# Kernel optimization log

Measured on AMD Instinct MI355X. Metric: run time of the kernel, lower is better.

The kernel has to match this reference:

```python
import jax, jax.numpy as jnp
import numpy as np

# ---- static config (eval-mode RPN, torchvision-style FPN) ----
LEVEL_HW = [(200, 200), (100, 100), (50, 50), (25, 25), (13, 13)]
STRIDES = [4, 8, 16, 32, 64]
SIZES = [32, 64, 128, 256, 512]
A = 3                      # anchors per location (3 aspect ratios)
IMG_H, IMG_W = 800, 800
PRE_N, POST_N = 1000, 1000 # pre/post NMS top-n (testing)
NMS_TH, SCORE_TH, MIN_SIZE = 0.7, 0.0, 1e-3
BBOX_CLIP = 4.135166556742356  # log(1000/16), BoxCoder clamp
NUM_PER_LEVEL = [A * h * w for h, w in LEVEL_HW]


def _make_anchors():
    ratios = np.array([0.5, 1.0, 2.0])
    hr = np.sqrt(ratios)
    wr = 1.0 / hr
    out = []
    for (H, W), size, stride in zip(LEVEL_HW, SIZES, STRIDES):
        ws, hs = wr * size, hr * size
        base = np.stack([-ws / 2, -hs / 2, ws / 2, hs / 2], axis=1)  # [A,4]
        sx = np.arange(W) * stride
        sy = np.arange(H) * stride
        yy, xx = np.meshgrid(sy, sx, indexing='ij')
        shifts = np.stack([xx.ravel(), yy.ravel(), xx.ravel(), yy.ravel()], axis=1)
        out.append((shifts[:, None, :] + base[None, :, :]).reshape(-1, 4))
    return np.concatenate(out, 0).astype(np.float32)


def setup_inputs() -> dict:
    key = jax.random.key(0)
    ks = jax.random.split(key, 10)
    N = 4
    inp = {}
    for i, (h, w) in enumerate(LEVEL_HW):
        inp[f'obj{i}'] = jax.random.normal(ks[i], (N, A, h, w), jnp.float32)
        inp[f'delta{i}'] = 0.5 * jax.random.normal(ks[5 + i], (N, 4 * A, h, w), jnp.float32)
    inp['anchors'] = jnp.asarray(_make_anchors())
    return inp


def _decode(deltas, anchors):
    # BoxCoder.decode with weights (1,1,1,1)
    wa = anchors[:, 2] - anchors[:, 0]
    ha = anchors[:, 3] - anchors[:, 1]
    cxa = anchors[:, 0] + 0.5 * wa
    cya = anchors[:, 1] + 0.5 * ha
    dx, dy = deltas[..., 0], deltas[..., 1]
    dw = jnp.minimum(deltas[..., 2], BBOX_CLIP)
    dh = jnp.minimum(deltas[..., 3], BBOX_CLIP)
    cx = dx * wa + cxa
    cy = dy * ha + cya
    w = jnp.exp(dw) * wa
    h = jnp.exp(dh) * ha
    return jnp.stack([cx - 0.5 * w, cy - 0.5 * h, cx + 0.5 * w, cy + 0.5 * h], -1)


def _box_iou(b1, b2):
    a1 = (b1[:, 2] - b1[:, 0]) * (b1[:, 3] - b1[:, 1])
    a2 = (b2[:, 2] - b2[:, 0]) * (b2[:, 3] - b2[:, 1])
    lt = jnp.maximum(b1[:, None, :2], b2[None, :, :2])
    rb = jnp.minimum(b1[:, None, 2:], b2[None, :, 2:])
    wh = jnp.clip(rb - lt, 0.0)
    inter = wh[..., 0] * wh[..., 1]
    return inter / (a1[:, None] + a2[None, :] - inter)


def _nms_keep(iou, valid):
    # greedy NMS over score-sorted boxes; valid marks surviving pre-filters
    K = iou.shape[0]
    def body(sup, i):
        k = valid[i] & jnp.logical_not(sup[i])
        sup = sup | (k & (iou[i] > NMS_TH))
        return sup, k
    _, keeps = jax.lax.scan(body, jnp.zeros(K, bool), jnp.arange(K))
    return keeps


def _per_image(boxes, scores, lvl):
    # clip_boxes_to_image
    x1 = jnp.clip(boxes[:, 0], 0.0, IMG_W)
    y1 = jnp.clip(boxes[:, 1], 0.0, IMG_H)
    x2 = jnp.clip(boxes[:, 2], 0.0, IMG_W)
    y2 = jnp.clip(boxes[:, 3], 0.0, IMG_H)
    boxes = jnp.stack([x1, y1, x2, y2], -1)
    # remove_small_boxes + score_thresh as validity mask
    valid = (x2 - x1 >= MIN_SIZE) & (y2 - y1 >= MIN_SIZE) & (scores >= SCORE_TH)
    ms = jnp.where(valid, scores, -1.0)
    order = jnp.argsort(-ms)
    b_s, v_s, s_s, l_s = boxes[order], valid[order], scores[order], lvl[order]
    # batched_nms trick: offset boxes by level so levels never overlap
    bn = jax.lax.stop_gradient(b_s) + (l_s.astype(boxes.dtype) * (IMG_W + 1.0))[:, None]
    keep = _nms_keep(_box_iou(bn, bn), v_s)
    sel_key = jnp.where(keep, jax.lax.stop_gradient(s_s), -1.0)
    topv, topi = jax.lax.top_k(sel_key, POST_N)
    m = topv > -0.5
    fb = jnp.where(m[:, None], b_s[topi], 0.0)
    fs = jnp.where(m, s_s[topi], 0.0)
    return fb, fs


def reference(obj0, obj1, obj2, obj3, obj4, delta0, delta1, delta2, delta3, delta4, anchors):
    objs = [obj0, obj1, obj2, obj3, obj4]
    dels = [delta0, delta1, delta2, delta3, delta4]
    N = obj0.shape[0]
    # permute_and_flatten + concat (objectness C=1)
    obj = jnp.concatenate([o.transpose(0, 2, 3, 1).reshape(N, -1) for o in objs], 1)
    dl = jnp.concatenate([
        d.reshape(N, A, 4, d.shape[2], d.shape[3]).transpose(0, 3, 4, 1, 2).reshape(N, -1, 4)
        for d in dels], 1)
    proposals = _decode(dl, anchors)  # [N, total, 4]
    levels = jnp.concatenate([jnp.full((n,), i, jnp.int32) for i, n in enumerate(NUM_PER_LEVEL)])
    # per-level top-k (static split)
    idxs, off = [], 0
    for n in NUM_PER_LEVEL:
        k = min(PRE_N, n)
        _, ti = jax.lax.top_k(obj[:, off:off + n], k)
        idxs.append(ti + off)
        off += n
    top_idx = jnp.concatenate(idxs, 1)  # [N, K]
    sel_obj = jnp.take_along_axis(obj, top_idx, 1)
    sel_lvl = levels[top_idx]
    sel_box = jnp.take_along_axis(proposals, top_idx[..., None], 1)
    scores = jax.nn.sigmoid(sel_obj)
    fb, fs = jax.vmap(_per_image)(sel_box, scores, sel_lvl)
    return fb, fs
```

## Files before the change

kernel.cpp:

```cpp
#include <hip/hip_runtime.h>
#include <cstdint>
#include <cstddef>

#define NLV 5
#define NIMG 4
#define NSEL 4507
#define TSEL (NIMG * NSEL)
#define POSTN 1000
#define TCAP 8192
#define TTCAP 2048
#define NHB 16
#define PBLK 64
#define PCH 1875

__device__ const int d_W[NLV]    = {200, 100, 50, 25, 13};
__device__ const int d_NL[NLV]   = {120000, 30000, 7500, 1875, 507};
__device__ const int d_KOFF[6]   = {0, 120000, 150000, 157500, 159375, 159882};
__device__ const int d_LOFF[6]   = {0, 1000, 2000, 3000, 4000, 4507};
__device__ const int d_KL[NLV]   = {1000, 1000, 1000, 1000, 507};

struct Ptrs {
    const float* obj[NLV];
    const float* del[NLV];
    const float* anch;
};

__device__ inline unsigned int dkey_of(float f) {
    unsigned int u = __float_as_uint(f);
    unsigned int mk = (u & 0x80000000u) ? ~u : (u | 0x80000000u);
    return ~mk;
}
__device__ inline float logit_from_dkey(unsigned int dk) {
    unsigned int mk = ~dk;
    unsigned int u = (mk & 0x80000000u) ? (mk & 0x7fffffffu) : ~mk;
    return __uint_as_float(u);
}

__global__ __launch_bounds__(256) void k_hist(Ptrs P, unsigned int* hist) {
    int l = blockIdx.y, n = blockIdx.z;
    int nl_sz = d_NL[l];
    if (d_KL[l] >= nl_sz) return;
    int nlid = n * NLV + l;
    __shared__ unsigned int h[2048];
    for (int i = threadIdx.x; i < 2048; i += 256) h[i] = 0;
    __syncthreads();
    const float* ob = P.obj[l] + (size_t)n * nl_sz;
    int chunk = (nl_sz + NHB - 1) / NHB;
    int beg = blockIdx.x * chunk;
    int end = min(beg + chunk, nl_sz);
    for (int t = beg + (int)threadIdx.x; t < end; t += 256)
        atomicAdd(&h[dkey_of(ob[t]) >> 21], 1u);
    __syncthreads();
    unsigned int* out = hist + ((size_t)nlid * NHB + blockIdx.x) * 2048;
    for (int i = threadIdx.x; i < 2048; i += 256) out[i] = h[i];
}

__global__ __launch_bounds__(1024) void k_thresh(const unsigned int* hist,
                                                 unsigned int* thr,
                                                 int* scnt, int* tcnt) {
    int nlid = blockIdx.x;
    int l = nlid % NLV;
    if (threadIdx.x == 0) { scnt[nlid] = 0; tcnt[nlid] = 0; }
    if (d_KL[l] >= d_NL[l]) return;
    int tid = threadIdx.x, w = tid >> 6, lane = tid & 63;
    __shared__ unsigned int wpre[16];
    const unsigned int* hb = hist + (size_t)nlid * NHB * 2048;
    unsigned int v0 = 0, v1 = 0;
    #pragma unroll
    for (int sh = 0; sh < NHB; ++sh) {
        v0 += hb[sh * 2048 + 2 * tid];
        v1 += hb[sh * 2048 + 2 * tid + 1];
    }
    unsigned int s = v0 + v1;
    unsigned int ps = s;
    #pragma unroll
    for (int d = 1; d < 64; d <<= 1) {
        unsigned int t2 = (unsigned int)__shfl_up((int)ps, d, 64);
        if (lane >= d) ps += t2;
    }
    if (lane == 63) wpre[w] = ps;
    __syncthreads();
    unsigned int base = 0;
    #pragma unroll
    for (int ww = 0; ww < 16; ++ww) if (ww < w) base += wpre[ww];
    unsigned int incl = base + ps;
    unsigned int target = (unsigned int)d_KL[l];
    unsigned int exc0 = incl - s, inc0 = incl - v1;
    unsigned int exc1 = inc0,    inc1 = incl;
    if (exc0 < target && target <= inc0) { thr[nlid * 2] = 2 * tid;     thr[nlid * 2 + 1] = exc0; }
    if (exc1 < target && target <= inc1) { thr[nlid * 2] = 2 * tid + 1; thr[nlid * 2 + 1] = exc1; }
}

__global__ __launch_bounds__(256) void k_pick(Ptrs P, const unsigned int* thr,
                                              int* scnt, int* tcnt,
                                              int* cg, float* cl,
                                              unsigned long long* tiebuf) {
    int l = blockIdx.y, n = blockIdx.z;
    int nl_sz = d_NL[l], kl = d_KL[l];
    int nlid = n * NLV + l;
    const float* ob = P.obj[l] + (size_t)n * nl_sz;
    int cbase = n * NSEL + d_LOFF[l];
    int koff = d_KOFF[l];
    int Wl = d_W[l], HW = Wl * Wl;
    int chunk = (nl_sz + PBLK - 1) / PBLK;
    int beg = blockIdx.x * chunk;
    int end = min(beg + chunk, nl_sz);
    int tid = threadIdx.x;

    if (kl >= nl_sz) {
        for (int t = beg + tid; t < end; t += 256) {
            int a = t / HW, rem = t - a * HW;
            int p = rem * 3 + a;
            cg[cbase + p] = koff + p;
            cl[cbase + p] = ob[t];
        }
        return;
    }
    __shared__ int sp[PCH];
    __shared__ float sl[PCH];
    __shared__ unsigned long long tb[PCH];
    __shared__ int nsel, ntie, sbase, tbase;
    if (tid == 0) { nsel = 0; ntie = 0; }
    __syncthreads();

    unsigned int b0 = thr[nlid * 2];
    for (int t = beg + tid; t < end; t += 256) {
        float lg = ob[t];
        unsigned int dk = dkey_of(lg);
        unsigned int bin = dk >> 21;
        if (bin < b0) {
            int pos = atomicAdd(&nsel, 1);
            int a = t / HW, rem = t - a * HW;
            sp[pos] = rem * 3 + a;
            sl[pos] = lg;
        } else if (bin == b0) {
            int pos = atomicAdd(&ntie, 1);
            int a = t / HW, rem = t - a * HW;
            tb[pos] = ((unsigned long long)dk << 17) |
                      (unsigned long long)(unsigned int)(rem * 3 + a);
        }
    }
    __syncthreads();
    if (tid == 0) {
        sbase = atomicAdd(&scnt[nlid], nsel);
        tbase = atomicAdd(&tcnt[nlid], ntie);
    }
    __syncthreads();
    int ns = nsel, nt = ntie, sb = sbase, tbs = tbase;
    for (int i = tid; i < ns; i += 256) {
        cg[cbase + sb + i] = koff + sp[i];
        cl[cbase + sb + i] = sl[i];
    }
    for (int i = tid; i < nt; i += 256) {
        int slot = tbs + i;
        if (slot < TCAP) tiebuf[(size_t)nlid * TCAP + slot] = tb[i];
    }
}

__global__ __launch_bounds__(1024) void k_tbs(Ptrs P, const unsigned int* thr,
                                              const int* tcnt,
                                              const unsigned long long* tiebuf,
                                              int* cg, float* cl,
                                              unsigned long long* skey,
                                              float4* sboxL, float* slogL,
                                              int* ccnt) {
#pragma clang fp contract(off)
    __shared__ union {
        struct { unsigned long long kk[TCAP];
                 unsigned long long tt[TTCAP];
                 unsigned int h2[2048]; } tie;
        struct { unsigned long long s[1024];
                 float4 bx[1024];
                 float lg[1024]; } srt;
    } U;
    __shared__ unsigned int wpre[16];
    __shared__ unsigned int s_b1, s_before;
    __shared__ int ctr, ttc;

    int l = blockIdx.x, n = blockIdx.y;
    int nl = n * NLV + l;
    int tid = threadIdx.x, w = tid >> 6, lane = tid & 63;
    int kl = d_KL[l], nl_sz = d_NL[l];
    int cbase = n * NSEL + d_LOFF[l];
    int koff = d_KOFF[l];

    if (kl < nl_sz) {
        int c = min(tcnt[nl], TCAP);
        unsigned int cnt_lt = thr[nl * 2 + 1];
        int need = kl - (int)cnt_lt;
        if (tid == 0) { ctr = 0; ttc = 0; }
        U.tie.h2[tid] = 0; U.tie.h2[tid + 1024] = 0;
        for (int i = tid; i < c; i += 1024) U.tie.kk[i] = tiebuf[(size_t)nl * TCAP + i];
        __syncthreads();
        for (int i = tid; i < c; i += 1024)
            atomicAdd(&U.tie.h2[(unsigned int)((U.tie.kk[i] >> 27) & 0x7ffull)], 1u);
        __syncthreads();
        unsigned int v0 = U.tie.h2[2 * tid], v1 = U.tie.h2[2 * tid + 1];
        unsigned int s = v0 + v1, ps = s;
        #pragma unroll
        for (int d = 1; d < 64; d <<= 1) {
            unsigned int t2 = (unsigned int)__shfl_up((int)ps, d, 64);
            if (lane >= d) ps += t2;
        }
        if (lane == 63) wpre[w] = ps;
        __syncthreads();
        unsigned int base = 0;
        #pragma unroll
        for (int ww = 0; ww < 16; ++ww) if (ww < w) base += wpre[ww];
        unsigned int incl = base + ps;
        unsigned int target = (unsigned int)need;
        unsigned int exc0 = incl - s, inc0 = incl - v1;
        unsigned int exc1 = inc0,    inc1 = incl;
        if (exc0 < target && target <= inc0) { s_b1 = 2 * tid;     s_before = exc0; }
        if (exc1 < target && target <= inc1) { s_b1 = 2 * tid + 1; s_before = exc1; }
        __syncthreads();
        unsigned int b1 = s_b1;
        int before = (int)s_before;
        for (int i = tid; i < c; i += 1024) {
            unsigned long long ki = U.tie.kk[i];
            unsigned int sb = (unsigned int)((ki >> 27) & 0x7ffull);
            if (sb < b1) {
                int slot = atomicAdd(&ctr, 1);
                int p = (int)(ki & 0x1ffffull);
                cg[cbase + (int)cnt_lt + slot] = koff + p;
                cl[cbase + (int)cnt_lt + slot] = logit_from_dkey((unsigned int)(ki >> 17));
            } else if (sb == b1) {
                int j = atomicAdd(&ttc, 1);
                if (j < TTCAP) U.tie.tt[j] = ki;
            }
        }
        __syncthreads();
        int c2 = min(ttc, TTCAP);
        int need2 = need - before;
        for (int i = tid; i < c2; i += 1024) {
            unsigned long long ki = U.tie.tt[i];
            int rank = 0;
            for (int j = 0; j < c2; ++j) rank += (U.tie.tt[j] < ki) ? 1 : 0;
            if (rank < need2) {
                int p = (int)(ki & 0x1ffffull);
                cg[cbase + (int)cnt_lt + before + rank] = koff + p;
                cl[cbase + (int)cnt_lt + before + rank] = logit_from_dkey((unsigned int)(ki >> 17));
            }
        }
    }
    __syncthreads();

    {
        int j = tid;
        unsigned long long key;
        float4 box;
        float lgv;
        if (j >= kl) {
            key = ((unsigned long long)0xFFFFFFFFu << 27) | (unsigned long long)j;
            box = make_float4(0.f, 0.f, 0.f, 0.f);
            lgv = 0.f;
        } else {
            int sidx = cbase + j;
            int gidx = cg[sidx];
            float lg = cl[sidx];
            int p = gidx - koff;
            int Wl = d_W[l];
            int HW = Wl * Wl;
            int a = p % 3, hw = p / 3;
            int hq = hw / Wl, wq = hw - hq * Wl;
            const float* dl = P.del[l];
            size_t dbase = (size_t)(n * 12 + a * 4) * HW + (size_t)hq * Wl + wq;
            float dx = dl[dbase], dy = dl[dbase + HW];
            float dw = dl[dbase + 2 * (size_t)HW], dh = dl[dbase + 3 * (size_t)HW];
            const float* an = P.anch + 4 * (size_t)gidx;
            float ax1 = an[0], ay1 = an[1], ax2 = an[2], ay2 = an[3];
            float wa = ax2 - ax1, ha = ay2 - ay1;
            float cxa = ax1 + 0.5f * wa, cya = ay1 + 0.5f * ha;
            const float CLIPC = (float)4.135166556742356;
            dw = fminf(dw, CLIPC); dh = fminf(dh, CLIPC);
            float cx = dx * wa + cxa;
            float cy = dy * ha + cya;
            float ww2 = expf(dw) * wa;
            float hh2 = expf(dh) * ha;
            float x1 = cx - 0.5f * ww2, y1 = cy - 0.5f * hh2;
            float x2 = cx + 0.5f * ww2, y2 = cy + 0.5f * hh2;
            x1 = fminf(fmaxf(x1, 0.0f), 800.0f);
            y1 = fminf(fmaxf(y1, 0.0f), 800.0f);
            x2 = fminf(fmaxf(x2, 0.0f), 800.0f);
            y2 = fminf(fmaxf(y2, 0.0f), 800.0f);
            bool valid = (x2 - x1 >= 1e-3f) && (y2 - y1 >= 1e-3f);
            box = make_float4(x1, y1, x2, y2);
            lgv = lg;
            unsigned int sk = valid ? dkey_of(lg) : 0xffffffffu;
            key = ((unsigned long long)sk << 27) |
                  ((unsigned long long)(unsigned int)p << 10) | (unsigned long long)j;
        }
        U.srt.s[j] = key;
        U.srt.bx[j] = box;
        U.srt.lg[j] = lgv;
    }
    __syncthreads();

    for (int k = 2; k <= 1024; k <<= 1) {
        for (int j2 = k >> 1; j2 > 0; j2 >>= 1) {
            if (tid < 512) {
                int i = ((tid & ~(j2 - 1)) << 1) | (tid & (j2 - 1));
                int ix = i | j2;
                bool up = ((i & k) == 0);
                unsigned long long A = U.srt.s[i], B = U.srt.s[ix];
                if ((A > B) == up) { U.srt.s[i] = B; U.srt.s[ix] = A; }
            }
            __syncthreads();
        }
    }
    {
        int e = tid;
        unsigned long long key = U.srt.s[e];
        int j = (int)(key & 0x3ffull);
        skey[(size_t)nl * 1024 + e] = key;
        sboxL[(size_t)nl * 1024 + e] = U.srt.bx[j];
        slogL[(size_t)nl * 1024 + e] = U.srt.lg[j];
        bool v = (key >> 27) != 0xFFFFFFFFull;
        bool vn = (e < 1023) ? ((U.srt.s[e + 1] >> 27) != 0xFFFFFFFFull) : false;
        if (e == 0 && !v) ccnt[nl] = 0;
        if (v && (e == 1023 || !vn)) ccnt[nl] = e + 1;
    }
}

__global__ __launch_bounds__(256) void k_mask(const float4* sboxL, const int* ccnt,
                                              unsigned long long* MT) {
#pragma clang fp contract(off)
    int n = blockIdx.z, l = blockIdx.y;
    int ci = blockIdx.x >> 4, cj = blockIdx.x & 15;
    int nl = n * NLV + l;
    int cnt = ccnt[nl];
    int nw = (cnt + 63) / 64;
    if (cj < ci || cj >= nw) return;
    __shared__ float4 bi[64], bj[64];
    int tid = threadIdx.x;
    float off = (float)l * 801.0f;
    if (tid < 64) {
        float4 b = sboxL[nl * 1024 + cj * 64 + tid];
        bj[tid] = make_float4(b.x + off, b.y + off, b.z + off, b.w + off);
    } else if (tid < 128) {
        float4 b = sboxL[nl * 1024 + ci * 64 + (tid - 64)];
        bi[tid - 64] = make_float4(b.x + off, b.y + off, b.z + off, b.w + off);
    }
    __syncthreads();
    int w = tid >> 6, lane = tid & 63;
    float4 B = bj[lane];
    float a2 = (B.z - B.x) * (B.w - B.y);
    unsigned long long* outp = MT + ((size_t)nl * 16 + cj) * 1024 + ci * 64;
    #pragma unroll
    for (int t = 0; t < 16; ++t) {
        int i = w * 16 + t;
        float4 A = bi[i];
        float a1 = (A.z - A.x) * (A.w - A.y);
        float ltx = fmaxf(A.x, B.x), lty = fmaxf(A.y, B.y);
        float rbx = fminf(A.z, B.z), rby = fminf(A.w, B.w);
        float wx = fmaxf(rbx - ltx, 0.f), wy = fmaxf(rby - lty, 0.f);
        float inter = wx * wy;
        float iou = inter / ((a1 + a2) - inter);
        unsigned long long word = __ballot(iou > 0.7f);
        if (lane == 0) outp[i] = word;
    }
}

__global__ __launch_bounds__(1024) void k_scan(const unsigned long long* MT,
                                               const int* ccnt,
                                               unsigned long long* keepL,
                                               float* out) {
    int l = blockIdx.x, n = blockIdx.y;
    int nl = n * NLV + l;
    int tid = threadIdx.x, w = tid >> 6, lane = tid & 63;
    __shared__ unsigned long long pendS[16];
    __shared__ unsigned long long defS[16];
    {
        int seg = POSTN / NLV;
        for (int i = tid; i < seg; i += 1024) {
            int idx = n * POSTN + l * seg + i;
            ((float4*)out)[idx] = make_float4(0.f, 0.f, 0.f, 0.f);
            out[NIMG * POSTN * 4 + idx] = 0.f;
        }
    }
    int cnt = ccnt[nl];
    int nw = (cnt + 63) / 64;

    const unsigned long long* base = MT + ((size_t)nl * 16 + w) * 1024;
    unsigned long long Dmask = 0;
    if (w < nw)
        Dmask = base[(size_t)w * 64 + lane] & ~((2ull << lane) - 1ull);
    unsigned long long rows[15];
    #pragma unroll
    for (int cc = 0; cc < 15; ++cc)
        rows[cc] = (cc < w && w < nw) ? base[(size_t)cc * 64 + lane] : 0ull;

    int nb = max(0, min(64, cnt - w * 64));
    unsigned long long pend_w = (nb == 64) ? ~0ull : ((nb > 0) ? ((1ull << nb) - 1ull) : 0ull);
    unsigned long long K_w = 0;
    if (lane == 0) pendS[w] = pend_w;
    __syncthreads();

    for (int round = 0; round < 1024; ++round) {
        unsigned long long any = 0;
        #pragma unroll
        for (int cc = 0; cc < 16; ++cc) any |= pendS[cc];
        if (!any) break;
        unsigned long long acc = ((pendS[w] >> lane) & 1ull) ? Dmask : 0ull;
        #pragma unroll
        for (int cc = 0; cc < 15; ++cc)
            if (cc < w) acc |= ((pendS[cc] >> lane) & 1ull) ? rows[cc] : 0ull;
        unsigned int vlo = (unsigned int)acc, vhi = (unsigned int)(acc >> 32);
        #pragma unroll
        for (int m = 1; m < 64; m <<= 1) {
            vlo |= (unsigned int)__shfl_xor((int)vlo, m, 64);
            vhi |= (unsigned int)__shfl_xor((int)vhi, m, 64);
        }
        unsigned long long sup = ((unsigned long long)vhi << 32) | (unsigned long long)vlo;
        unsigned long long def_w = pend_w & ~sup;
        K_w |= def_w;
        if (lane == 0) defS[w] = def_w;
        __syncthreads();
        unsigned long long acc2 = ((defS[w] >> lane) & 1ull) ? Dmask : 0ull;
        #pragma unroll
        for (int cc = 0; cc < 15; ++cc)
            if (cc < w) acc2 |= ((defS[cc] >> lane) & 1ull) ? rows[cc] : 0ull;
        unsigned int rlo = (unsigned int)acc2, rhi = (unsigned int)(acc2 >> 32);
        #pragma unroll
        for (int m = 1; m < 64; m <<= 1) {
            rlo |= (unsigned int)__shfl_xor((int)rlo, m, 64);
            rhi |= (unsigned int)__shfl_xor((int)rhi, m, 64);
        }
        unsigned long long rem = ((unsigned long long)rhi << 32) | (unsigned long long)rlo;
        pend_w &= ~def_w & ~rem;
        if (lane == 0) pendS[w] = pend_w;
        __syncthreads();
    }
    if (lane == 0) keepL[nl * 16 + w] = K_w;
}

__global__ __launch_bounds__(1024) void k_rank(const unsigned long long* skey,
                                               const unsigned long long* keepL,
                                               const int* ccnt,
                                               const float4* sboxL, const float* slogL,
                                               float* out) {
    int l = blockIdx.x, n = blockIdx.y;
    int tid = threadIdx.x;
    __shared__ unsigned long long KS[NLV][1024];
    __shared__ unsigned long long kd[NLV][16];
    __shared__ int kpre[NLV][17];
    __shared__ int lcnt[NLV];
    for (int e = tid; e < NLV * 1024; e += 1024)
        ((unsigned long long*)KS)[e] = skey[(size_t)n * NLV * 1024 + e];
    if (tid < NLV * 16) ((unsigned long long*)kd)[tid] = keepL[n * NLV * 16 + tid];
    if (tid < NLV) lcnt[tid] = ccnt[n * NLV + tid];
    __syncthreads();
    if (tid < NLV) {
        int run = 0;
        for (int q = 0; q < 16; ++q) { kpre[tid][q] = run; run += (int)__popcll(kd[tid][q]); }
        kpre[tid][16] = run;
    }
    __syncthreads();
    int i = tid;
    if (i >= lcnt[l]) return;
    int q = i >> 6, b = i & 63;
    if (!((kd[l][q] >> b) & 1ull)) return;
    int rank = kpre[l][q] + (int)__popcll(kd[l][q] & ((1ull << b) - 1ull));
    unsigned int sk = (unsigned int)(KS[l][i] >> 27);
    for (int l2 = 0; l2 < NLV; ++l2) {
        if (l2 == l) continue;
        int c2 = lcnt[l2];
        unsigned long long bound = (l2 < l)
            ? (((unsigned long long)sk + 1ull) << 27)
            : ((unsigned long long)sk << 27);
        int lo = 0, hi = c2;
        while (lo < hi) {
            int mid = (lo + hi) >> 1;
            if (KS[l2][mid] < bound) lo = mid + 1; else hi = mid;
        }
        int mq = lo >> 6, mb = lo & 63;
        rank += kpre[l2][mq] + (mb ? (int)__popcll(kd[l2][mq] & ((1ull << mb) - 1ull)) : 0);
    }
    if (rank < POSTN) {
        ((float4*)out)[n * POSTN + rank] = sboxL[(size_t)(n * NLV + l) * 1024 + i];
        float lg = slogL[(size_t)(n * NLV + l) * 1024 + i];
        out[NIMG * POSTN * 4 + n * POSTN + rank] = 1.0f / (1.0f + expf(-lg));
    }
}

extern "C" void kernel_launch(void* const* d_in, const int* in_sizes, int n_in,
                              void* d_out, int out_size, void* d_ws, size_t ws_size,
                              hipStream_t stream) {
    Ptrs P;
    bool interleaved = (in_sizes[1] == 4 * in_sizes[0]);
    for (int i = 0; i < NLV; ++i) {
        if (interleaved) {
            P.obj[i] = (const float*)d_in[2 * i];
            P.del[i] = (const float*)d_in[2 * i + 1];
        } else {
            P.obj[i] = (const float*)d_in[i];
            P.del[i] = (const float*)d_in[NLV + i];
        }
    }
    P.anch = (const float*)d_in[10];

    char* w = (char*)d_ws;
    size_t off = 0;
    auto alloc = [&](size_t bytes) {
        void* p = w + off;
        off = (off + bytes + 255) & ~(size_t)255;
        return p;
    };
    const size_t NLT = (size_t)NIMG * NLV * 1024;
    unsigned int* hist = (unsigned int*)alloc((size_t)NIMG * NLV * NHB * 2048 * 4);
    int* scnt = (int*)alloc(256);
    int* tcnt = (int*)alloc(256);
    unsigned int* thr = (unsigned int*)alloc((size_t)NIMG * NLV * 2 * 4);
    unsigned long long* tiebuf = (unsigned long long*)alloc((size_t)NIMG * NLV * TCAP * 8);
    int* cg      = (int*)alloc((size_t)TSEL * 4);
    float* cl    = (float*)alloc((size_t)TSEL * 4);
    unsigned long long* skey = (unsigned long long*)alloc(NLT * 8);
    float4* sboxL = (float4*)alloc(NLT * 16);
    float* slogL  = (float*)alloc(NLT * 4);
    int* ccnt    = (int*)alloc((size_t)NIMG * NLV * 4);
    unsigned long long* keepL = (unsigned long long*)alloc((size_t)NIMG * NLV * 16 * 8);
    unsigned long long* MT = (unsigned long long*)alloc((size_t)NIMG * NLV * 16 * 1024 * 8);
    (void)ws_size; (void)n_in;

    k_hist<<<dim3(NHB, NLV, NIMG), 256, 0, stream>>>(P, hist);
    k_thresh<<<NIMG * NLV, 1024, 0, stream>>>(hist, thr, scnt, tcnt);
    k_pick<<<dim3(PBLK, NLV, NIMG), 256, 0, stream>>>(P, thr, scnt, tcnt, cg, cl, tiebuf);
    k_tbs<<<dim3(NLV, NIMG), 1024, 0, stream>>>(P, thr, tcnt, tiebuf, cg, cl,
                                                skey, sboxL, slogL, ccnt);
    k_mask<<<dim3(256, NLV, NIMG), 256, 0, stream>>>(sboxL, ccnt, MT);
    k_scan<<<dim3(NLV, NIMG), 1024, 0, stream>>>(MT, ccnt, keepL, (float*)d_out);
    k_rank<<<dim3(NLV, NIMG), 1024, 0, stream>>>(skey, keepL, ccnt, sboxL, slogL, (float*)d_out);
}
```

Measured before the change: 159.7 us.

## Fuse seven RPN kernels into one cooperative persistent kernel with grid syncs

Replaces the chain of seven kernel launches (histogram, threshold, pick, tie-break sort, IoU mask, NMS scan, rank) with a single cooperative kernel of 256 blocks x 1024 threads that separates the phases with grid-wide syncs. The goal is to remove per-launch overhead and the gaps between small dependent kernels. Work is remapped onto fixed block counts: the histogram packs four sub-blocks per block, pick runs in five passes, and the IoU mask uses a loop over triangle tiles. The old multi-launch path is kept as a fallback if the cooperative launch fails. The cost is that grid syncs add their own latency, and the 1024-thread blocks with a large shared-memory union may limit occupancy in the phases that do most of the work.

```diff
diff --git a/kernel.cpp b/kernel.cpp
--- a/kernel.cpp
+++ b/kernel.cpp
@@ -1,6 +1,9 @@
 #include <hip/hip_runtime.h>
+#include <hip/hip_cooperative_groups.h>
 #include <cstdint>
 #include <cstddef>
+
+namespace cgrp = cooperative_groups;
 
 #define NLV 5
 #define NIMG 4
@@ -12,6 +15,8 @@
 #define NHB 16
 #define PBLK 64
 #define PCH 1875
+#define NTRI 136
+#define GRID 256
 
 __device__ const int d_W[NLV]    = {200, 100, 50, 25, 13};
 __device__ const int d_NL[NLV]   = {120000, 30000, 7500, 1875, 507};
@@ -34,6 +39,450 @@
     unsigned int mk = ~dk;
     unsigned int u = (mk & 0x80000000u) ? (mk & 0x7fffffffu) : ~mk;
     return __uint_as_float(u);
+}
+
+__global__ __launch_bounds__(1024) void k_all(Ptrs P,
+        unsigned int* hist, int* scnt, int* tcnt, unsigned int* thr,
+        unsigned long long* tiebuf, int* cgv, float* clv,
+        unsigned long long* skey, float4* sboxL, float* slogL,
+        int* ccnt, unsigned long long* keepL, unsigned long long* MT,
+        float* out) {
+#pragma clang fp contract(off)
+    cgrp::grid_group gg = cgrp::this_grid();
+    int bid = blockIdx.x, tid = threadIdx.x;
+    int w = tid >> 6, lane = tid & 63;
+
+    __shared__ union {
+        unsigned int h4[4][2048];
+        struct { int sp[PCH]; float sl[PCH];
+                 unsigned long long tb[PCH]; } pk;
+        struct { unsigned long long kk[TCAP];
+                 unsigned long long tt[TTCAP];
+                 unsigned int h2[2048]; } tie;
+        struct { unsigned long long s[1024]; float4 bx[1024];
+                 float lg[1024]; } srt;
+        struct { float4 bi[64]; float4 bj[64]; } mk;
+        unsigned long long KS[NLV][1024];
+    } U;
+    __shared__ unsigned int wpre[16];
+    __shared__ unsigned int s_b1, s_before;
+    __shared__ int ctr, ttc;
+    __shared__ int nselS, ntieS, sbaseS, tbaseS;
+    __shared__ unsigned long long pendS[16], defS[16];
+    __shared__ unsigned long long kd[NLV][16];
+    __shared__ int kpre[NLV][17];
+    __shared__ int lcnt[NLV];
+
+    {
+        for (int i = tid; i < 4 * 2048; i += 1024) ((unsigned int*)U.h4)[i] = 0;
+        __syncthreads();
+        int g = bid * 4 + (tid >> 8);
+        int tsub = tid & 255;
+        int u = ((g % 3) == 0 && (g / 3) < 320) ? (g / 3) : -1;
+        int nlid = -1, l = 0, n = 0, sub = 0;
+        if (u >= 0) {
+            nlid = u >> 4; sub = u & 15;
+            n = nlid / NLV; l = nlid % NLV;
+            if (d_KL[l] >= d_NL[l]) nlid = -1;
+        }
+        if (nlid >= 0) {
+            int nl_sz = d_NL[l];
+            const float* ob = P.obj[l] + (size_t)n * nl_sz;
+            int chunk = (nl_sz + NHB - 1) / NHB;
+            int beg = sub * chunk, end = min(beg + chunk, nl_sz);
+            unsigned int* hh = U.h4[tid >> 8];
+            for (int t = beg + tsub; t < end; t += 256)
+                atomicAdd(&hh[dkey_of(ob[t]) >> 21], 1u);
+        }
+        __syncthreads();
+        if (nlid >= 0) {
+            unsigned int* hh = U.h4[tid >> 8];
+            unsigned int* op = hist + ((size_t)nlid * NHB + sub) * 2048;
+            for (int i = tsub; i < 2048; i += 256) op[i] = hh[i];
+        }
+        if (bid >= GRID - 16) {
+            int z = (bid - (GRID - 16)) * 1024 + tid;
+            if (z < NIMG * POSTN) {
+                ((float4*)out)[z] = make_float4(0.f, 0.f, 0.f, 0.f);
+                out[NIMG * POSTN * 4 + z] = 0.f;
+            }
+        }
+    }
+    gg.sync();
+
+    if (bid < NIMG * NLV) {
+        int nlid = bid, l = nlid % NLV;
+        if (tid == 0) { scnt[nlid] = 0; tcnt[nlid] = 0; }
+        if (d_KL[l] < d_NL[l]) {
+            const unsigned int* hb = hist + (size_t)nlid * NHB * 2048;
+            unsigned int v0 = 0, v1 = 0;
+            #pragma unroll
+            for (int sh = 0; sh < NHB; ++sh) {
+                v0 += hb[sh * 2048 + 2 * tid];
+                v1 += hb[sh * 2048 + 2 * tid + 1];
+            }
+            unsigned int s = v0 + v1, ps = s;
+            #pragma unroll
+            for (int d = 1; d < 64; d <<= 1) {
+                unsigned int t2 = (unsigned int)__shfl_up((int)ps, d, 64);
+                if (lane >= d) ps += t2;
+            }
+            if (lane == 63) wpre[w] = ps;
+            __syncthreads();
+            unsigned int base = 0;
+            #pragma unroll
+            for (int ww = 0; ww < 16; ++ww) if (ww < w) base += wpre[ww];
+            unsigned int incl = base + ps;
+            unsigned int target = (unsigned int)d_KL[l];
+            unsigned int exc0 = incl - s, inc0 = incl - v1;
+            unsigned int exc1 = inc0,    inc1 = incl;
+            if (exc0 < target && target <= inc0) { thr[nlid * 2] = 2 * tid;     thr[nlid * 2 + 1] = exc0; }
+            if (exc1 < target && target <= inc1) { thr[nlid * 2] = 2 * tid + 1; thr[nlid * 2 + 1] = exc1; }
+        }
+    }
+    gg.sync();
+
+    for (int pass = 0; pass < 5; ++pass) {
+        int unit = pass * GRID + bid;
+        int nlid = unit >> 6, pb = unit & 63;
+        int n = nlid / NLV, l = nlid % NLV;
+        int nl_sz = d_NL[l], kl = d_KL[l];
+        const float* ob = P.obj[l] + (size_t)n * nl_sz;
+        int cbase = n * NSEL + d_LOFF[l];
+        int koff = d_KOFF[l];
+        int Wl = d_W[l], HW = Wl * Wl;
+        int chunk = (nl_sz + PBLK - 1) / PBLK;
+        int beg = pb * chunk, end = min(beg + chunk, nl_sz);
+
+        if (kl >= nl_sz) {
+            for (int t = beg + tid; t < end; t += 1024) {
+                int a = t / HW, rem = t - a * HW;
+                int p = rem * 3 + a;
+                cgv[cbase + p] = koff + p;
+                clv[cbase + p] = ob[t];
+            }
+            continue;
+        }
+        if (tid == 0) { nselS = 0; ntieS = 0; }
+        __syncthreads();
+        unsigned int b0 = thr[nlid * 2];
+        for (int t = beg + tid; t < end; t += 1024) {
+            float lg = ob[t];
+            unsigned int dk = dkey_of(lg);
+            unsigned int bin = dk >> 21;
+            if (bin < b0) {
+                int pos = atomicAdd(&nselS, 1);
+                int a = t / HW, rem = t - a * HW;
+                U.pk.sp[pos] = rem * 3 + a;
+                U.pk.sl[pos] = lg;
+            } else if (bin == b0) {
+                int pos = atomicAdd(&ntieS, 1);
+                int a = t / HW, rem = t - a * HW;
+                U.pk.tb[pos] = ((unsigned long long)dk << 17) |
+                               (unsigned long long)(unsigned int)(rem * 3 + a);
+            }
+        }
+        __syncthreads();
+        if (tid == 0) {
+            sbaseS = atomicAdd(&scnt[nlid], nselS);
+            tbaseS = atomicAdd(&tcnt[nlid], ntieS);
+        }
+        __syncthreads();
+        int ns = nselS, nt2 = ntieS, sb = sbaseS, tb2 = tbaseS;
+        for (int i = tid; i < ns; i += 1024) {
+            cgv[cbase + sb + i] = koff + U.pk.sp[i];
+            clv[cbase + sb + i] = U.pk.sl[i];
+        }
+        for (int i = tid; i < nt2; i += 1024) {
+            int slot = tb2 + i;
+            if (slot < TCAP) tiebuf[(size_t)nlid * TCAP + slot] = U.pk.tb[i];
+        }
+    }
+    gg.sync();
+
+    if (bid < NIMG * NLV) {
+        int nlid = bid;
+        int n = nlid / NLV, l = nlid % NLV;
+        int kl = d_KL[l], nl_sz = d_NL[l];
+        int cbase = n * NSEL + d_LOFF[l];
+        int koff = d_KOFF[l];
+
+        if (kl < nl_sz) {
+            int c = min(tcnt[nlid], TCAP);
+            unsigned int cnt_lt = thr[nlid * 2 + 1];
+            int need = kl - (int)cnt_lt;
+            if (tid == 0) { ctr = 0; ttc = 0; }
+            U.tie.h2[tid] = 0; U.tie.h2[tid + 1024] = 0;
+            for (int i = tid; i < c; i += 1024) U.tie.kk[i] = tiebuf[(size_t)nlid * TCAP + i];
+            __syncthreads();
+            for (int i = tid; i < c; i += 1024)
+                atomicAdd(&U.tie.h2[(unsigned int)((U.tie.kk[i] >> 27) & 0x7ffull)], 1u);
+            __syncthreads();
+            unsigned int v0 = U.tie.h2[2 * tid], v1 = U.tie.h2[2 * tid + 1];
+            unsigned int s = v0 + v1, ps = s;
+            #pragma unroll
+            for (int d = 1; d < 64; d <<= 1) {
+                unsigned int t2 = (unsigned int)__shfl_up((int)ps, d, 64);
+                if (lane >= d) ps += t2;
+            }
+            if (lane == 63) wpre[w] = ps;
+            __syncthreads();
+            unsigned int base = 0;
+            #pragma unroll
+            for (int ww = 0; ww < 16; ++ww) if (ww < w) base += wpre[ww];
+            unsigned int incl = base + ps;
+            unsigned int target = (unsigned int)need;
+            unsigned int exc0 = incl - s, inc0 = incl - v1;
+            unsigned int exc1 = inc0,    inc1 = incl;
+            if (exc0 < target && target <= inc0) { s_b1 = 2 * tid;     s_before = exc0; }
+            if (exc1 < target && target <= inc1) { s_b1 = 2 * tid + 1; s_before = exc1; }
+            __syncthreads();
+            unsigned int b1 = s_b1;
+            int before = (int)s_before;
+            for (int i = tid; i < c; i += 1024) {
+                unsigned long long ki = U.tie.kk[i];
+                unsigned int sb = (unsigned int)((ki >> 27) & 0x7ffull);
+                if (sb < b1) {
+                    int slot = atomicAdd(&ctr, 1);
+                    int p = (int)(ki & 0x1ffffull);
+                    cgv[cbase + (int)cnt_lt + slot] = koff + p;
+                    clv[cbase + (int)cnt_lt + slot] = logit_from_dkey((unsigned int)(ki >> 17));
+                } else if (sb == b1) {
+                    int j = atomicAdd(&ttc, 1);
+                    if (j < TTCAP) U.tie.tt[j] = ki;
+                }
+            }
+            __syncthreads();
+            int c2 = min(ttc, TTCAP);
+            int need2 = need - before;
+            for (int i = tid; i < c2; i += 1024) {
+                unsigned long long ki = U.tie.tt[i];
+                int rank = 0;
+                for (int j = 0; j < c2; ++j) rank += (U.tie.tt[j] < ki) ? 1 : 0;
+                if (rank < need2) {
+                    int p = (int)(ki & 0x1ffffull);
+                    cgv[cbase + (int)cnt_lt + before + rank] = koff + p;
+                    clv[cbase + (int)cnt_lt + before + rank] = logit_from_dkey((unsigned int)(ki >> 17));
+                }
+            }
+        }
+        __syncthreads();
+
+        {
+            int j = tid;
+            unsigned long long key;
+            float4 box;
+            float lgv;
+            if (j >= kl) {
+                key = ((unsigned long long)0xFFFFFFFFu << 27) | (unsigned long long)j;
+                box = make_float4(0.f, 0.f, 0.f, 0.f);
+                lgv = 0.f;
+            } else {
+                int sidx = cbase + j;
+                int gidx = cgv[sidx];
+                float lg = clv[sidx];
+                int p = gidx - koff;
+                int Wl = d_W[l];
+                int HW = Wl * Wl;
+                int a = p % 3, hw = p / 3;
+                int hq = hw / Wl, wq = hw - hq * Wl;
+                const float* dl = P.del[l];
+                size_t dbase = (size_t)(n * 12 + a * 4) * HW + (size_t)hq * Wl + wq;
+                float dx = dl[dbase], dy = dl[dbase + HW];
+                float dw = dl[dbase + 2 * (size_t)HW], dh = dl[dbase + 3 * (size_t)HW];
+                const float* an = P.anch + 4 * (size_t)gidx;
+                float ax1 = an[0], ay1 = an[1], ax2 = an[2], ay2 = an[3];
+                float wa = ax2 - ax1, ha = ay2 - ay1;
+                float cxa = ax1 + 0.5f * wa, cya = ay1 + 0.5f * ha;
+                const float CLIPC = (float)4.135166556742356;
+                dw = fminf(dw, CLIPC); dh = fminf(dh, CLIPC);
+                float cx = dx * wa + cxa;
+                float cy = dy * ha + cya;
+                float ww2 = expf(dw) * wa;
+                float hh2 = expf(dh) * ha;
+                float x1 = cx - 0.5f * ww2, y1 = cy - 0.5f * hh2;
+                float x2 = cx + 0.5f * ww2, y2 = cy + 0.5f * hh2;
+                x1 = fminf(fmaxf(x1, 0.0f), 800.0f);
+                y1 = fminf(fmaxf(y1, 0.0f), 800.0f);
+                x2 = fminf(fmaxf(x2, 0.0f), 800.0f);
+                y2 = fminf(fmaxf(y2, 0.0f), 800.0f);
+                bool valid = (x2 - x1 >= 1e-3f) && (y2 - y1 >= 1e-3f);
+                box = make_float4(x1, y1, x2, y2);
+                lgv = lg;
+                unsigned int sk = valid ? dkey_of(lg) : 0xffffffffu;
+                key = ((unsigned long long)sk << 27) |
+                      ((unsigned long long)(unsigned int)p << 10) | (unsigned long long)j;
+            }
+            U.srt.s[j] = key;
+            U.srt.bx[j] = box;
+            U.srt.lg[j] = lgv;
+        }
+        __syncthreads();
+
+        for (int k = 2; k <= 1024; k <<= 1) {
+            for (int j2 = k >> 1; j2 > 0; j2 >>= 1) {
+                if (tid < 512) {
+                    int i = ((tid & ~(j2 - 1)) << 1) | (tid & (j2 - 1));
+                    int ix = i | j2;
+                    bool up = ((i & k) == 0);
+                    unsigned long long A = U.srt.s[i], B = U.srt.s[ix];
+                    if ((A > B) == up) { U.srt.s[i] = B; U.srt.s[ix] = A; }
+                }
+                __syncthreads();
+            }
+        }
+        {
+            int e = tid;
+            unsigned long long key = U.srt.s[e];
+            int j = (int)(key & 0x3ffull);
+            skey[(size_t)nlid * 1024 + e] = key;
+            sboxL[(size_t)nlid * 1024 + e] = U.srt.bx[j];
+            slogL[(size_t)nlid * 1024 + e] = U.srt.lg[j];
+            bool v = (key >> 27) != 0xFFFFFFFFull;
+            bool vn = (e < 1023) ? ((U.srt.s[e + 1] >> 27) != 0xFFFFFFFFull) : false;
+            if (e == 0 && !v) ccnt[nlid] = 0;
+            if (v && (e == 1023 || !vn)) ccnt[nlid] = e + 1;
+        }
+    }
+    gg.sync();
+
+    for (int T = bid; T < NIMG * NLV * NTRI; T += GRID) {
+        int nl = T / NTRI, t136 = T - nl * NTRI;
+        int cnt = ccnt[nl];
+        int nw = (cnt + 63) / 64;
+        int cj = 0;
+        while (((cj + 1) * (cj + 2)) >> 1 <= t136) ++cj;
+        int ci = t136 - ((cj * (cj + 1)) >> 1);
+        if (cj >= nw) continue;
+        int l = nl % NLV;
+        float off = (float)l * 801.0f;
+        __syncthreads();
+        if (tid < 64) {
+            float4 b = sboxL[(size_t)nl * 1024 + cj * 64 + tid];
+            U.mk.bj[tid] = make_float4(b.x + off, b.y + off, b.z + off, b.w + off);
+        } else if (tid < 128) {
+            float4 b = sboxL[(size_t)nl * 1024 + ci * 64 + (tid - 64)];
+            U.mk.bi[tid - 64] = make_float4(b.x + off, b.y + off, b.z + off, b.w + off);
+        }
+        __syncthreads();
+        float4 B = U.mk.bj[lane];
+        float a2 = (B.z - B.x) * (B.w - B.y);
+        unsigned long long* outp = MT + ((size_t)nl * 16 + cj) * 1024 + ci * 64;
+        #pragma unroll
+        for (int t = 0; t < 4; ++t) {
+            int i = w * 4 + t;
+            float4 A = U.mk.bi[i];
+            float a1 = (A.z - A.x) * (A.w - A.y);
+            float ltx = fmaxf(A.x, B.x), lty = fmaxf(A.y, B.y);
+            float rbx = fminf(A.z, B.z), rby = fminf(A.w, B.w);
+            float wx = fmaxf(rbx - ltx, 0.f), wy = fmaxf(rby - lty, 0.f);
+            float inter = wx * wy;
+            float iou = inter / ((a1 + a2) - inter);
+            unsigned long long word = __ballot(iou > 0.7f);
+            if (lane == 0) outp[i] = word;
+        }
+    }
+    gg.sync();
+
+    if (bid < NIMG * NLV) {
+        int nl = bid;
+        int cnt = ccnt[nl];
+        int nw = (cnt + 63) / 64;
+        const unsigned long long* base = MT + ((size_t)nl * 16 + w) * 1024;
+        unsigned long long Dmask = 0;
+        if (w < nw)
+            Dmask = base[(size_t)w * 64 + lane] & ~((2ull << lane) - 1ull);
+        unsigned long long rows[15];
+        #pragma unroll
+        for (int cc = 0; cc < 15; ++cc)
+            rows[cc] = (cc < w && w < nw) ? base[(size_t)cc * 64 + lane] : 0ull;
+
+        int nb = max(0, min(64, cnt - w * 64));
+        unsigned long long pend_w = (nb == 64) ? ~0ull : ((nb > 0) ? ((1ull << nb) - 1ull) : 0ull);
+        unsigned long long K_w = 0;
+        if (lane == 0) pendS[w] = pend_w;
+        __syncthreads();
+
+        for (int round = 0; round < 1024; ++round) {
+            unsigned long long any = 0;
+            #pragma unroll
+            for (int cc = 0; cc < 16; ++cc) any |= pendS[cc];
+            if (!any) break;
+            unsigned long long acc = ((pendS[w] >> lane) & 1ull) ? Dmask : 0ull;
+            #pragma unroll
+            for (int cc = 0; cc < 15; ++cc)
+                if (cc < w) acc |= ((pendS[cc] >> lane) & 1ull) ? rows[cc] : 0ull;
+            unsigned int vlo = (unsigned int)acc, vhi = (unsigned int)(acc >> 32);
+            #pragma unroll
+            for (int m = 1; m < 64; m <<= 1) {
+                vlo |= (unsigned int)__shfl_xor((int)vlo, m, 64);
+                vhi |= (unsigned int)__shfl_xor((int)vhi, m, 64);
+            }
+            unsigned long long sup = ((unsigned long long)vhi << 32) | (unsigned long long)vlo;
+            unsigned long long def_w = pend_w & ~sup;
+            K_w |= def_w;
+            if (lane == 0) defS[w] = def_w;
+            __syncthreads();
+            unsigned long long acc2 = ((defS[w] >> lane) & 1ull) ? Dmask : 0ull;
+            #pragma unroll
+            for (int cc = 0; cc < 15; ++cc)
+                if (cc < w) acc2 |= ((defS[cc] >> lane) & 1ull) ? rows[cc] : 0ull;
+            unsigned int rlo = (unsigned int)acc2, rhi = (unsigned int)(acc2 >> 32);
+            #pragma unroll
+            for (int m = 1; m < 64; m <<= 1) {
+                rlo |= (unsigned int)__shfl_xor((int)rlo, m, 64);
+                rhi |= (unsigned int)__shfl_xor((int)rhi, m, 64);
+            }
+            unsigned long long rem = ((unsigned long long)rhi << 32) | (unsigned long long)rlo;
+            pend_w &= ~def_w & ~rem;
+            if (lane == 0) pendS[w] = pend_w;
+            __syncthreads();
+        }
+        if (lane == 0) keepL[nl * 16 + w] = K_w;
+    }
+    gg.sync();
+
+    if (bid < NIMG * NLV) {
+        int l = bid % NLV, n = bid / NLV;
+        for (int e = tid; e < NLV * 1024; e += 1024)
+            ((unsigned long long*)U.KS)[e] = skey[(size_t)n * NLV * 1024 + e];
+        if (tid < NLV * 16) ((unsigned long long*)kd)[tid] = keepL[n * NLV * 16 + tid];
+        if (tid < NLV) lcnt[tid] = ccnt[n * NLV + tid];
+        __syncthreads();
+        if (tid < NLV) {
+            int run = 0;
+            for (int q = 0; q < 16; ++q) { kpre[tid][q] = run; run += (int)__popcll(kd[tid][q]); }
+            kpre[tid][16] = run;
+        }
+        __syncthreads();
+        int i = tid;
+        if (i < lcnt[l]) {
+            int q = i >> 6, b = i & 63;
+            if ((kd[l][q] >> b) & 1ull) {
+                int rank = kpre[l][q] + (int)__popcll(kd[l][q] & ((1ull << b) - 1ull));
+                unsigned int sk = (unsigned int)(U.KS[l][i] >> 27);
+                for (int l2 = 0; l2 < NLV; ++l2) {
+                    if (l2 == l) continue;
+                    int c2 = lcnt[l2];
+                    unsigned long long bound = (l2 < l)
+                        ? (((unsigned long long)sk + 1ull) << 27)
+                        : ((unsigned long long)sk << 27);
+                    int lo = 0, hi = c2;
+                    while (lo < hi) {
+                        int mid = (lo + hi) >> 1;
+                        if (U.KS[l2][mid] < bound) lo = mid + 1; else hi = mid;
+                    }
+                    int mq = lo >> 6, mb = lo & 63;
+                    rank += kpre[l2][mq] + (mb ? (int)__popcll(kd[l2][mq] & ((1ull << mb) - 1ull)) : 0);
+                }
+                if (rank < POSTN) {
+                    ((float4*)out)[n * POSTN + rank] = sboxL[(size_t)(n * NLV + l) * 1024 + i];
+                    float lg = slogL[(size_t)(n * NLV + l) * 1024 + i];
+                    out[NIMG * POSTN * 4 + n * POSTN + rank] = 1.0f / (1.0f + expf(-lg));
+                }
+            }
+        }
+    }
 }
 
 __global__ __launch_bounds__(256) void k_hist(Ptrs P, unsigned int* hist) {
@@ -93,7 +542,7 @@
 
 __global__ __launch_bounds__(256) void k_pick(Ptrs P, const unsigned int* thr,
                                               int* scnt, int* tcnt,
-                                              int* cg, float* cl,
+                                              int* cgv, float* clv,
                                               unsigned long long* tiebuf) {
     int l = blockIdx.y, n = blockIdx.z;
     int nl_sz = d_NL[l], kl = d_KL[l];
@@ -111,8 +560,8 @@
         for (int t = beg + tid; t < end; t += 256) {
             int a = t / HW, rem = t - a * HW;
             int p = rem * 3 + a;
-            cg[cbase + p] = koff + p;
-            cl[cbase + p] = ob[t];
+            cgv[cbase + p] = koff + p;
+            clv[cbase + p] = ob[t];
         }
         return;
     }
@@ -148,8 +597,8 @@
     __syncthreads();
     int ns = nsel, nt = ntie, sb = sbase, tbs = tbase;
     for (int i = tid; i < ns; i += 256) {
-        cg[cbase + sb + i] = koff + sp[i];
-        cl[cbase + sb + i] = sl[i];
+        cgv[cbase + sb + i] = koff + sp[i];
+        clv[cbase + sb + i] = sl[i];
     }
     for (int i = tid; i < nt; i += 256) {
         int slot = tbs + i;
@@ -160,7 +609,7 @@
 __global__ __launch_bounds__(1024) void k_tbs(Ptrs P, const unsigned int* thr,
                                               const int* tcnt,
                                               const unsigned long long* tiebuf,
-                                              int* cg, float* cl,
+                                              int* cgv, float* clv,
                                               unsigned long long* skey,
                                               float4* sboxL, float* slogL,
                                               int* ccnt) {
@@ -222,8 +671,8 @@
             if (sb < b1) {
                 int slot = atomicAdd(&ctr, 1);
                 int p = (int)(ki & 0x1ffffull);
-                cg[cbase + (int)cnt_lt + slot] = koff + p;
-                cl[cbase + (int)cnt_lt + slot] = logit_from_dkey((unsigned int)(ki >> 17));
+                cgv[cbase + (int)cnt_lt + slot] = koff + p;
+                clv[cbase + (int)cnt_lt + slot] = logit_from_dkey((unsigned int)(ki >> 17));
             } else if (sb == b1) {
                 int j = atomicAdd(&ttc, 1);
                 if (j < TTCAP) U.tie.tt[j] = ki;
@@ -238,8 +687,8 @@
             for (int j = 0; j < c2; ++j) rank += (U.tie.tt[j] < ki) ? 1 : 0;
             if (rank < need2) {
                 int p = (int)(ki & 0x1ffffull);
-                cg[cbase + (int)cnt_lt + before + rank] = koff + p;
-                cl[cbase + (int)cnt_lt + before + rank] = logit_from_dkey((unsigned int)(ki >> 17));
+                cgv[cbase + (int)cnt_lt + before + rank] = koff + p;
+                clv[cbase + (int)cnt_lt + before + rank] = logit_from_dkey((unsigned int)(ki >> 17));
             }
         }
     }
@@ -256,8 +705,8 @@
             lgv = 0.f;
         } else {
             int sidx = cbase + j;
-            int gidx = cg[sidx];
-            float lg = cl[sidx];
+            int gidx = cgv[sidx];
+            float lg = clv[sidx];
             int p = gidx - koff;
             int Wl = d_W[l];
             int HW = Wl * Wl;
@@ -512,22 +961,32 @@
     int* tcnt = (int*)alloc(256);
     unsigned int* thr = (unsigned int*)alloc((size_t)NIMG * NLV * 2 * 4);
     unsigned long long* tiebuf = (unsigned long long*)alloc((size_t)NIMG * NLV * TCAP * 8);
-    int* cg      = (int*)alloc((size_t)TSEL * 4);
-    float* cl    = (float*)alloc((size_t)TSEL * 4);
+    int* cgv     = (int*)alloc((size_t)TSEL * 4);
+    float* clv   = (float*)alloc((size_t)TSEL * 4);
     unsigned long long* skey = (unsigned long long*)alloc(NLT * 8);
     float4* sboxL = (float4*)alloc(NLT * 16);
     float* slogL  = (float*)alloc(NLT * 4);
     int* ccnt    = (int*)alloc((size_t)NIMG * NLV * 4);
     unsigned long long* keepL = (unsigned long long*)alloc((size_t)NIMG * NLV * 16 * 8);
     unsigned long long* MT = (unsigned long long*)alloc((size_t)NIMG * NLV * 16 * 1024 * 8);
+    float* outp = (float*)d_out;
     (void)ws_size; (void)n_in;
 
-    k_hist<<<dim3(NHB, NLV, NIMG), 256, 0, stream>>>(P, hist);
-    k_thresh<<<NIMG * NLV, 1024, 0, stream>>>(hist, thr, scnt, tcnt);
-    k_pick<<<dim3(PBLK, NLV, NIMG), 256, 0, stream>>>(P, thr, scnt, tcnt, cg, cl, tiebuf);
-    k_tbs<<<dim3(NLV, NIMG), 1024, 0, stream>>>(P, thr, tcnt, tiebuf, cg, cl,
-                                                skey, sboxL, slogL, ccnt);
-    k_mask<<<dim3(256, NLV, NIMG), 256, 0, stream>>>(sboxL, ccnt, MT);
-    k_scan<<<dim3(NLV, NIMG), 1024, 0, stream>>>(MT, ccnt, keepL, (float*)d_out);
-    k_rank<<<dim3(NLV, NIMG), 1024, 0, stream>>>(skey, keepL, ccnt, sboxL, slogL, (float*)d_out);
-}
+    void* args[] = { (void*)&P, (void*)&hist, (void*)&scnt, (void*)&tcnt,
+                     (void*)&thr, (void*)&tiebuf, (void*)&cgv, (void*)&clv,
+                     (void*)&skey, (void*)&sboxL, (void*)&slogL, (void*)&ccnt,
+                     (void*)&keepL, (void*)&MT, (void*)&outp };
+    hipError_t e = hipLaunchCooperativeKernel((const void*)k_all, dim3(GRID),
+                                              dim3(1024), args, 0, stream);
+    if (e != hipSuccess) {
+        (void)hipGetLastError();
+        k_hist<<<dim3(NHB, NLV, NIMG), 256, 0, stream>>>(P, hist);
+        k_thresh<<<NIMG * NLV, 1024, 0, stream>>>(hist, thr, scnt, tcnt);
+        k_pick<<<dim3(PBLK, NLV, NIMG), 256, 0, stream>>>(P, thr, scnt, tcnt, cgv, clv, tiebuf);
+        k_tbs<<<dim3(NLV, NIMG), 1024, 0, stream>>>(P, thr, tcnt, tiebuf, cgv, clv,
+                                                    skey, sboxL, slogL, ccnt);
+        k_mask<<<dim3(256, NLV, NIMG), 256, 0, stream>>>(sboxL, ccnt, MT);
+        k_scan<<<dim3(NLV, NIMG), 1024, 0, stream>>>(MT, ccnt, keepL, outp);
+        k_rank<<<dim3(NLV, NIMG), 1024, 0, stream>>>(skey, keepL, ccnt, sboxL, slogL, outp);
+    }
+}
```

Result: slower. 337.0 us (+111.0%).
